# Kernel optimization log

Measured on AMD Instinct MI355X. Metric: run time of the kernel, lower is better.

Reference implementation:

```python
import jax, jax.numpy as jnp
import numpy as np

# NSA hyperparams (match init_kwargs)
D_BLK = 64    # d: block stride
L_CMP = 64    # compression block length (== d -> non-overlapping blocks)
L_SLC = 64    # selection block length (== l_cmp == d -> P_slc = P_cmp)
BQ = 64       # block_size_q
TOPK = 16     # slc_top_k
WL, WR = 512, 0  # sliding window (left, right)


def _nsa_forward(q, k, v, w_k, b_k, w_v, b_v, w_gate, b_gate, seqlen):
    S, qh, dim = q.shape
    kv = k.shape[1]
    H = qh // kv
    b = S // seqlen          # number of equal-length packed sequences
    s = seqlen
    scale = dim ** -0.5
    f32 = jnp.float32

    # [b, s, kv, H, e]: q head g*H+h belongs to kv head g (repeat_interleave layout)
    q5 = q.reshape(b, s, kv, H, dim)
    k3 = k.reshape(b, s, kv, dim)
    v3 = v.reshape(b, s, kv, dim)

    # ---- block compression (extract_blocks + cmp_linear over block length) ----
    n_blk = s // D_BLK
    kb = k.reshape(b, n_blk, D_BLK, kv, dim)
    vb = v.reshape(b, n_blk, D_BLK, kv, dim)
    K_cmp = jnp.einsum('bntke,t->bnke', kb, w_k) + b_k[0]
    V_cmp = jnp.einsum('bntke,t->bnke', vb, w_v) + b_v[0]

    # ---- compressed attention (per sequence, fp32 softmax) ----
    sc = jnp.einsum('bqkhe,bnke->bkhqn', q5, K_cmp).astype(f32) * scale
    P = jax.nn.softmax(sc, axis=-1)
    out_cmp = jnp.einsum('bkhqn,bnke->bqkhe', P.astype(q.dtype), V_cmp)

    # ---- selection scores: pool P over q-blocks and GQA groups, then top-k ----
    nqb = s // BQ
    pooled = P.reshape(b, kv, H, nqb, BQ, n_blk).sum(axis=(2, 4))  # [b,kv,nqb,n_blk]
    idx = jax.lax.top_k(pooled, TOPK)[1]                            # [b,kv,nqb,TOPK]

    # gather selected K/V blocks (shared by all queries in a q-block / GQA group)
    kb2 = jnp.transpose(kb, (0, 3, 1, 2, 4))  # [b,kv,n_blk,l,e]
    vb2 = jnp.transpose(vb, (0, 3, 1, 2, 4))
    gather = jax.vmap(jax.vmap(lambda blocks, i: blocks[i]))
    K_sel = gather(kb2, idx)  # [b,kv,nqb,TOPK,l,e]
    V_sel = gather(vb2, idx)

    # ---- selected-block attention ----
    qblk = q5.reshape(b, nqb, BQ, kv, H, dim)
    sc2 = jnp.einsum('bnckhe,bkntle->bkhnctl', qblk, K_sel).astype(f32) * scale
    sc2 = sc2.reshape(b, kv, H, nqb, BQ, TOPK * L_SLC)
    P2 = jax.nn.softmax(sc2, axis=-1).astype(q.dtype)
    out_slc = jnp.einsum('bkhncm,bknme->bnckhe', P2,
                         V_sel.reshape(b, kv, nqb, TOPK * L_SLC, dim))
    out_slc = out_slc.reshape(b, s, kv, H, dim)

    # ---- sliding-window attention (window_size=(WL, WR), non-causal flag) ----
    sw = jnp.einsum('bikhe,bjke->bkhij', q5, k3).astype(f32) * scale
    i = jnp.arange(s)[:, None]
    j = jnp.arange(s)[None, :]
    valid = (j >= i - WL) & (j <= i + WR)
    sw = jnp.where(valid, sw, -jnp.inf)
    Pw = jax.nn.softmax(sw, axis=-1).astype(q.dtype)
    out_win = jnp.einsum('bkhij,bjke->bikhe', Pw, v3)

    # ---- gated fusion of the three branches ----
    gate = jax.nn.sigmoid(jnp.einsum('bqkhe,ec->bqkhc', q5, w_gate) + b_gate)
    out = (gate[..., 0:1] * out_cmp
           + gate[..., 1:2] * out_slc
           + gate[..., 2:3] * out_win)
    return out.reshape(S, qh, dim)


def setup_inputs() -> dict:
    key = jax.random.key(0)
    ks = jax.random.split(key, 9)
    S, qh, kvh, dim = 4096, 8, 2, 128
    inp = {
        'q': jax.random.normal(ks[0], (S, qh, dim), jnp.float32),
        'k': jax.random.normal(ks[1], (S, kvh, dim), jnp.float32),
        'v': jax.random.normal(ks[2], (S, kvh, dim), jnp.float32),
        'w_k': jax.random.normal(ks[3], (L_CMP,), jnp.float32) * (L_CMP ** -0.5),
        'b_k': jax.random.normal(ks[4], (1,), jnp.float32) * 0.02,
        'w_v': jax.random.normal(ks[5], (L_CMP,), jnp.float32) * (L_CMP ** -0.5),
        'b_v': jax.random.normal(ks[6], (1,), jnp.float32) * 0.02,
        'w_gate': jax.random.normal(ks[7], (dim, 3), jnp.float32) * (dim ** -0.5),
        'b_gate': jax.random.normal(ks[8], (3,), jnp.float32) * 0.02,
        'seqlen': 2048,
    }
    return inp


def reference(q, k, v, w_k, b_k, w_v, b_v, w_gate, b_gate, seqlen):
    return _nsa_forward(q, k, v, w_k, b_k, w_v, b_v, w_gate, b_gate, seqlen)
```

## Files before the change

kernel.cpp:

```cpp
#include <hip/hip_runtime.h>
#include <hip/hip_bf16.h>


#define SEQ   2048
#define NB    2
#define KV    2
#define NH    4
#define QH    8
#define DIM   128
#define NBLK  32
#define NQB   32
#define NTOP  16
#define SCALE 0.08838834764831845f
#define QSC   0.12751831795244785f
#define VP    72
#define VSU   68

typedef unsigned short ushort_t;
using bf16x8 = __attribute__((ext_vector_type(8))) short;
using f32x4  = __attribute__((ext_vector_type(4))) float;

__device__ float g_slcB[4194304];
__device__ float g_winB[4194304];
__device__ float g_cp[1048576];
__device__ float g_mlg[4][65536];

__device__ __forceinline__ unsigned pkbf(float a, float b){
  union { __hip_bfloat162 h; unsigned u; } cv;
  cv.h = __float22bfloat162_rn(make_float2(a, b));
  return cv.u;
}
__device__ __forceinline__ ushort_t b16(float f){
  union { float f; unsigned i; } x; x.f = f;
  unsigned r = x.i + 0x7fffu + ((x.i >> 16) & 1u);
  return (ushort_t)(r >> 16);
}
__device__ __forceinline__ float fb(ushort_t h){
  union { unsigned i; float f; } x; x.i = ((unsigned)h) << 16;
  return x.f;
}

__global__ __launch_bounds__(256) void prep_k(
    const float* __restrict__ k, const float* __restrict__ v,
    const float* __restrict__ w_k, const float* __restrict__ b_k,
    const float* __restrict__ w_v, const float* __restrict__ b_v,
    ushort_t* __restrict__ Kb, ushort_t* __restrict__ VT,
    float* __restrict__ Kc, float* __restrict__ Vc)
{
  int blk = blockIdx.x;
  int db = blk & 1, rb = (blk >> 1) & 31, bbg = blk >> 6;
  int bb = bbg >> 1, g = bbg & 1;
  int tid = threadIdx.x;
  __shared__ ushort_t T[64*VP];
  __shared__ float wks[64], wvs[64];
  __shared__ float accK[16][64], accV[16][64];

  if (tid < 64){ wks[tid] = w_k[tid]; wvs[tid] = w_v[tid]; }
  __syncthreads();

  float4 sk = {0,0,0,0}, sv = {0,0,0,0};
  for (int jj = 0; jj < 4; ++jj){
    int i = tid + jj*256;
    int r = i >> 4, ds = i & 15;
    size_t src = ((size_t)(bb*SEQ + rb*64 + r)*KV + g)*DIM + db*64 + ds*4;
    float4 kx = *(const float4*)(k + src);
    float4 vx = *(const float4*)(v + src);
    uint2 kk; kk.x = pkbf(kx.x,kx.y); kk.y = pkbf(kx.z,kx.w);
    size_t rowb = ((size_t)bbg*SEQ + rb*64 + r)*DIM*2;
    int swz = (db*128 + ds*8) ^ ((r & 7) << 4);
    *(uint2*)((char*)Kb + rowb + swz) = kk;
    unsigned v01 = pkbf(vx.x,vx.y), v23 = pkbf(vx.z,vx.w);
    T[(ds*4+0)*VP + r] = (ushort_t)(v01 & 0xffffu);
    T[(ds*4+1)*VP + r] = (ushort_t)(v01 >> 16);
    T[(ds*4+2)*VP + r] = (ushort_t)(v23 & 0xffffu);
    T[(ds*4+3)*VP + r] = (ushort_t)(v23 >> 16);
    float a = wks[r], b = wvs[r];
    sk.x += a*kx.x; sk.y += a*kx.y; sk.z += a*kx.z; sk.w += a*kx.w;
    sv.x += b*vx.x; sv.y += b*vx.y; sv.z += b*vx.z; sv.w += b*vx.w;
  }
  *(float4*)&accK[tid>>4][(tid&15)*4] = sk;
  *(float4*)&accV[tid>>4][(tid&15)*4] = sv;
  __syncthreads();

  for (int jj = 0; jj < 4; ++jj){
    int i = tid + jj*256;
    int d = i >> 4, seg = i & 15;
    uint2 u = *(uint2*)&T[d*VP + seg*4];
    size_t rowb = ((size_t)bbg*DIM + db*64 + d)*SEQ*2;
    int swz = (seg*8) ^ ((d & 7) << 4);
    *(uint2*)((char*)VT + rowb + rb*128 + swz) = u;
  }

  size_t obase = ((size_t)(bbg*NBLK + rb))*DIM + db*64;
  if (tid < 64){
    float s = 0.f;
#pragma unroll
    for (int i = 0; i < 16; ++i) s += accK[i][tid];
    Kc[obase + tid] = s + b_k[0];
  } else if (tid < 128){
    int d = tid - 64;
    float s = 0.f;
#pragma unroll
    for (int i = 0; i < 16; ++i) s += accV[i][d];
    Vc[obase + d] = s + b_v[0];
  }
}

__global__ __launch_bounds__(512, 2) void attn_k(
    const float* __restrict__ q, const ushort_t* __restrict__ Kb,
    const ushort_t* __restrict__ VT, const float* __restrict__ Kc,
    const float* __restrict__ w_gate, const float* __restrict__ b_gate,
    float* __restrict__ slcbuf, float* __restrict__ out)
{
  int idx = blockIdx.x;
  int x = idx & 7, low = idx & 1, u = idx >> 3;
  int bbg = x >> 1;
  int j = u*2 + low;
  int role = j >> 6;
  int sub  = (j >> 5) & 1;
  int qb = j & 31;
  int bb = bbg >> 1, g = bbg & 1;

  int tid = threadIdx.x;
  int lane = tid & 63, w = tid >> 6;
  int quad = lane >> 4, l15 = lane & 15;
  int h = w & 3, qh2 = w >> 2;
  int xr = (l15 & 7) << 4;

  __shared__ ushort_t Ks[64*128];
  __shared__ ushort_t Vs[128*VSU];
  __shared__ ushort_t Ps[256*VP];
  __shared__ float pw[8][NBLK];
  __shared__ float gbuf[256];
  __shared__ int   idxs[NTOP];

  if (role == 0){
    int key = tid >> 4, dq = tid & 15;
    const float* kcs = Kc + ((size_t)bbg*NBLK + key)*DIM + dq*8;
    float4 f0 = *(const float4*)kcs, f1 = *(const float4*)(kcs + 4);
    float fe[8] = {f0.x,f0.y,f0.z,f0.w,f1.x,f1.y,f1.z,f1.w};
    union { ushort_t u[8]; uint4 v; } hi, lo;
#pragma unroll
    for (int e = 0; e < 8; ++e){
      ushort_t hh = b16(fe[e]);
      hi.u[e] = hh; lo.u[e] = b16(fe[e] - fb(hh));
    }
    int off = (dq*16) ^ ((key & 7) << 4);
    *(uint4*)((char*)&Ks[0] + key*256 + off) = hi.v;
    *(uint4*)((char*)&Ks[0] + (key+32)*256 + off) = lo.v;
  }

  const float* qrow0 = q + ((size_t)(bb*SEQ + qb*64 + qh2*32 + l15)*QH + g*NH + h)*DIM;
  const float* qrow1 = qrow0 + (size_t)16*QH*DIM;
  int gcol = 1 + role;
  bf16x8 qfrag0[4], qfrag1[4], qlo0[4], qlo1[4];
  float gp0 = 0.f, gp1 = 0.f, gc0 = 0.f, gc1 = 0.f;
#pragma unroll
  for (int kc = 0; kc < 4; ++kc){
    int d0 = kc*32 + quad*8;
    float4 a0 = *(const float4*)(qrow0 + d0);
    float4 a1 = *(const float4*)(qrow0 + d0 + 4);
    float4 b0 = *(const float4*)(qrow1 + d0);
    float4 b1 = *(const float4*)(qrow1 + d0 + 4);
    float qa[8] = {a0.x,a0.y,a0.z,a0.w,a1.x,a1.y,a1.z,a1.w};
    float qc[8] = {b0.x,b0.y,b0.z,b0.w,b1.x,b1.y,b1.z,b1.w};
#pragma unroll
    for (int jj = 0; jj < 8; ++jj){
      float wg = w_gate[(d0+jj)*3 + gcol];
      gp0 += qa[jj]*wg; gp1 += qc[jj]*wg;
    }
    if (role == 0){
#pragma unroll
      for (int jj = 0; jj < 8; ++jj){
        float w0 = w_gate[(d0+jj)*3];
        gc0 += qa[jj]*w0; gc1 += qc[jj]*w0;
      }
      union { ushort_t u[8]; bf16x8 v; } h0, l0, h1, l1;
#pragma unroll
      for (int e = 0; e < 8; ++e){
        float s0f = qa[e]*QSC; ushort_t hh0 = b16(s0f);
        h0.u[e] = hh0; l0.u[e] = b16(s0f - fb(hh0));
        float s1f = qc[e]*QSC; ushort_t hh1 = b16(s1f);
        h1.u[e] = hh1; l1.u[e] = b16(s1f - fb(hh1));
      }
      qfrag0[kc] = h0.v; qlo0[kc] = l0.v;
      qfrag1[kc] = h1.v; qlo1[kc] = l1.v;
    } else {
      union { unsigned uu[4]; bf16x8 v8; } t0, t1;
#pragma unroll
      for (int p2 = 0; p2 < 4; ++p2){
        t0.uu[p2] = pkbf(qa[2*p2]*QSC, qa[2*p2+1]*QSC);
        t1.uu[p2] = pkbf(qc[2*p2]*QSC, qc[2*p2+1]*QSC);
      }
      qfrag0[kc] = t0.v8; qfrag1[kc] = t1.v8;
    }
  }
  gp0 += __shfl_xor(gp0,16); gp0 += __shfl_xor(gp0,32);
  gp1 += __shfl_xor(gp1,16); gp1 += __shfl_xor(gp1,32);
  if (quad == 0){
    gbuf[w*32 + l15]      = 1.f/(1.f + __expf(-(gp0 + b_gate[gcol])));
    gbuf[w*32 + 16 + l15] = 1.f/(1.f + __expf(-(gp1 + b_gate[gcol])));
  }
  float g0c0 = 0.f, g0c1 = 0.f;
  if (role == 0){
    gc0 += __shfl_xor(gc0,16); gc0 += __shfl_xor(gc0,32);
    gc1 += __shfl_xor(gc1,16); gc1 += __shfl_xor(gc1,32);
    g0c0 = 1.f/(1.f + __expf(-(gc0 + b_gate[0])));
    g0c1 = 1.f/(1.f + __expf(-(gc1 + b_gate[0])));
  }
  __syncthreads();
  float gl0[4], gl1[4];
#pragma unroll
  for (int r = 0; r < 4; ++r){
    gl0[r] = gbuf[w*32 + quad*4 + r];
    gl1[r] = gbuf[w*32 + 16 + quad*4 + r];
  }

  const f32x4 zero4 = {0.f,0.f,0.f,0.f};

  if (role == 0){
    f32x4 c0[2], c1[2];
    c0[0]=zero4; c0[1]=zero4; c1[0]=zero4; c1[1]=zero4;
#pragma unroll
    for (int kc = 0; kc < 4; ++kc){
#pragma unroll
      for (int nt = 0; nt < 2; ++nt){
        bf16x8 ah = *(bf16x8*)((char*)&Ks[0] + (nt*16 + l15)*256
                               + ((kc*64 + quad*16) ^ xr));
        bf16x8 al = *(bf16x8*)((char*)&Ks[0] + (nt*16 + l15 + 32)*256
                               + ((kc*64 + quad*16) ^ xr));
        c0[nt] = __builtin_amdgcn_mfma_f32_16x16x32_bf16(ah, qfrag0[kc], c0[nt], 0, 0, 0);
        c0[nt] = __builtin_amdgcn_mfma_f32_16x16x32_bf16(ah, qlo0[kc],   c0[nt], 0, 0, 0);
        c0[nt] = __builtin_amdgcn_mfma_f32_16x16x32_bf16(al, qfrag0[kc], c0[nt], 0, 0, 0);
        c1[nt] = __builtin_amdgcn_mfma_f32_16x16x32_bf16(ah, qfrag1[kc], c1[nt], 0, 0, 0);
        c1[nt] = __builtin_amdgcn_mfma_f32_16x16x32_bf16(ah, qlo1[kc],   c1[nt], 0, 0, 0);
        c1[nt] = __builtin_amdgcn_mfma_f32_16x16x32_bf16(al, qfrag1[kc], c1[nt], 0, 0, 0);
      }
    }
    float mx0 = -INFINITY, mx1 = -INFINITY;
#pragma unroll
    for (int nt = 0; nt < 2; ++nt)
#pragma unroll
      for (int r = 0; r < 4; ++r){
        mx0 = fmaxf(mx0, c0[nt][r]); mx1 = fmaxf(mx1, c1[nt][r]);
      }
    mx0 = fmaxf(mx0, __shfl_xor(mx0,16)); mx0 = fmaxf(mx0, __shfl_xor(mx0,32));
    mx1 = fmaxf(mx1, __shfl_xor(mx1,16)); mx1 = fmaxf(mx1, __shfl_xor(mx1,32));
    float s0 = 0.f, s1 = 0.f;
#pragma unroll
    for (int nt = 0; nt < 2; ++nt)
#pragma unroll
      for (int r = 0; r < 4; ++r){
        float p0v = exp2f(c0[nt][r] - mx0); c0[nt][r] = p0v; s0 += p0v;
        float p1v = exp2f(c1[nt][r] - mx1); c1[nt][r] = p1v; s1 += p1v;
      }
    s0 += __shfl_xor(s0,16); s0 += __shfl_xor(s0,32);
    s1 += __shfl_xor(s1,16); s1 += __shfl_xor(s1,32);
    float ip0 = 1.f/s0, ip1 = 1.f/s1;
    if (sub == 0){
      float ig0 = g0c0*ip0, ig1 = g0c1*ip1;
      size_t rh0 = ((size_t)(bb*SEQ + qb*64 + qh2*32 + l15)*QH + g*NH + h);
      size_t rh1 = rh0 + (size_t)16*QH;
#pragma unroll
      for (int nt = 0; nt < 2; ++nt)
#pragma unroll
        for (int r = 0; r < 4; ++r){
          int key = nt*16 + quad*4 + r;
          g_cp[rh0*NBLK + key] = c0[nt][r]*ig0;
          g_cp[rh1*NBLK + key] = c1[nt][r]*ig1;
        }
    }
#pragma unroll
    for (int nt = 0; nt < 2; ++nt)
#pragma unroll
      for (int r = 0; r < 4; ++r){
        float t = c0[nt][r]*ip0 + c1[nt][r]*ip1;
        t += __shfl_xor(t,1); t += __shfl_xor(t,2);
        t += __shfl_xor(t,4); t += __shfl_xor(t,8);
        if (l15 == 0) pw[w][nt*16 + quad*4 + r] = t;
      }
    __syncthreads();
    if (tid < 64){
      int n = lane;
      float val = -INFINITY;
      if (n < NBLK){
        float sm = 0.f;
#pragma unroll
        for (int w2 = 0; w2 < 8; ++w2) sm += pw[w2][n];
        val = sm;
      }
      int idxv = n;
      for (int kk = 2; kk <= 32; kk <<= 1){
        for (int jj2 = kk >> 1; jj2 > 0; jj2 >>= 1){
          float pv = __shfl_xor(val, jj2);
          int   pi = __shfl_xor(idxv, jj2);
          bool lower = (lane & jj2) == 0;
          bool desc  = (lane & kk) == 0;
          bool iwin  = (val > pv) || (val == pv && idxv < pi);
          bool keep  = (lower == desc) ? iwin : !iwin;
          if (!keep){ val = pv; idxv = pi; }
        }
      }
      if (lane < NTOP) idxs[lane] = idxv;
    }
    __syncthreads();
  }

  const ushort_t* kbase  = Kb + (size_t)bbg*SEQ*DIM;
  const ushort_t* vtbase = VT + (size_t)bbg*DIM*SEQ;

  int kb0 = (qb >= 8) ? (qb - 8) : 0;
  int N   = qb - kb0 + 1;
  int nph0 = (N + 1) >> 1;
  int nph = (role == 0) ? 8 : (sub ? (N - nph0) : nph0);
  int tb  = kb0 + sub*nph0;
  int qi0 = qh2*32 + l15, qi1 = qi0 + 16;

  float m10 = -INFINITY, l10 = 0.f, m11 = -INFINITY, l11 = 0.f;
  f32x4 oacc0[8], oacc1[8];
#pragma unroll
  for (int dt = 0; dt < 8; ++dt){ oacc0[dt] = zero4; oacc1[dt] = zero4; }

  uint2 kr[4], vr[4];
  auto loadKV = [&](int rowbase){
#pragma unroll
    for (int jj = 0; jj < 4; ++jj){
      int unit = tid + jj*512;
      int krow = unit >> 5, kseg = unit & 31;
      kr[jj] = *(const uint2*)(kbase + (size_t)(rowbase + krow)*DIM + kseg*4);
      int vd = unit >> 4, vsg = unit & 15;
      vr[jj] = *(const uint2*)(vtbase + (size_t)vd*SEQ + rowbase + vsg*4);
    }
  };
  auto writeKV = [&](){
#pragma unroll
    for (int jj = 0; jj < 4; ++jj){
      int unit = tid + jj*512;
      int krow = unit >> 5, kseg = unit & 31;
      *(uint2*)&Ks[krow*128 + kseg*4] = kr[jj];
      int vd = unit >> 4, vsg = unit & 15;
      *(uint2*)&Vs[vd*VSU + vsg*4] = vr[jj];
    }
  };

  if (nph > 0){
    int r0 = (role == 0) ? idxs[sub*8]*64 : tb*64;
    loadKV(r0);
    writeKV();
    __syncthreads();

    for (int t = 0; t < nph; ++t){
      int kb = (role == 0) ? idxs[sub*8 + t] : (tb + t);
      if (t+1 < nph){
        int rn = (role == 0) ? idxs[sub*8 + t + 1]*64 : (tb + t + 1)*64;
        loadKV(rn);
      }
      __builtin_amdgcn_sched_barrier(0);

      f32x4 sacc0[4], sacc1[4];
#pragma unroll
      for (int nt = 0; nt < 4; ++nt){ sacc0[nt] = zero4; sacc1[nt] = zero4; }
      __builtin_amdgcn_s_setprio(1);
#pragma unroll
      for (int kc = 0; kc < 4; ++kc){
#pragma unroll
        for (int nt = 0; nt < 4; ++nt){
          bf16x8 a = *(bf16x8*)((char*)&Ks[0] + (nt*16 + l15)*256
                                + ((kc*64 + quad*16) ^ xr));
          sacc0[nt] = __builtin_amdgcn_mfma_f32_16x16x32_bf16(a, qfrag0[kc], sacc0[nt], 0, 0, 0);
          sacc1[nt] = __builtin_amdgcn_mfma_f32_16x16x32_bf16(a, qfrag1[kc], sacc1[nt], 0, 0, 0);
        }
      }
      __builtin_amdgcn_s_setprio(0);

      bool mlow  = (role == 1) && (qb >= 8) && (kb == qb - 8);
      bool mhigh = (role == 1) && (kb == qb);
      bool domask = mlow | mhigh;

      auto softmax_qt = [&](f32x4* sc2, float& m1r, float& l1r, int qi_l,
                            bool& skipped) -> float {
        if (domask){
#pragma unroll
          for (int nt = 0; nt < 4; ++nt)
#pragma unroll
            for (int r = 0; r < 4; ++r){
              int key = nt*16 + quad*4 + r;
              bool valid = (!mlow || key >= qi_l) && (!mhigh || key <= qi_l);
              sc2[nt][r] = valid ? sc2[nt][r] : -INFINITY;
            }
        }
        float mnt[4];
#pragma unroll
        for (int nt = 0; nt < 4; ++nt)
          mnt[nt] = fmaxf(fmaxf(sc2[nt][0], sc2[nt][1]),
                          fmaxf(sc2[nt][2], sc2[nt][3]));
        float mx = fmaxf(fmaxf(mnt[0], mnt[1]), fmaxf(mnt[2], mnt[3]));
        mx = fmaxf(mx, __shfl_xor(mx, 16));
        mx = fmaxf(mx, __shfl_xor(mx, 32));
        float al = 1.f;
        skipped = __all(mx <= m1r + 8.f);
        if (!skipped){
          float mn = fmaxf(m1r, mx);
          al = exp2f(m1r - mn);
          m1r = mn;
        }
        float snt[4];
#pragma unroll
        for (int nt = 0; nt < 4; ++nt){
          float p0 = exp2f(sc2[nt][0] - m1r);
          float p1 = exp2f(sc2[nt][1] - m1r);
          float p2 = exp2f(sc2[nt][2] - m1r);
          float p3 = exp2f(sc2[nt][3] - m1r);
          sc2[nt][0] = p0; sc2[nt][1] = p1; sc2[nt][2] = p2; sc2[nt][3] = p3;
          snt[nt] = (p0 + p1) + (p2 + p3);
        }
        float s0 = (snt[0] + snt[1]) + (snt[2] + snt[3]);
        s0 += __shfl_xor(s0, 16);
        s0 += __shfl_xor(s0, 32);
        l1r = l1r*al + s0;
        return al;
      };
      bool sk0, sk1;
      float al0 = softmax_qt(sacc0, m10, l10, qi0, sk0);
      float al1 = softmax_qt(sacc1, m11, l11, qi1, sk1);

#pragma unroll
      for (int nt = 0; nt < 4; ++nt){
        uint2 p0, p1;
        p0.x = pkbf(sacc0[nt][0], sacc0[nt][1]);
        p0.y = pkbf(sacc0[nt][2], sacc0[nt][3]);
        p1.x = pkbf(sacc1[nt][0], sacc1[nt][1]);
        p1.y = pkbf(sacc1[nt][2], sacc1[nt][3]);
        *(uint2*)&Ps[(w*32 + l15)*VP + nt*16 + quad*4] = p0;
        *(uint2*)&Ps[(w*32 + 16 + l15)*VP + nt*16 + quad*4] = p1;
      }

      if (!sk0){
        float ar[4];
#pragma unroll
        for (int r = 0; r < 4; ++r) ar[r] = __shfl(al0, quad*4 + r);
#pragma unroll
        for (int dt = 0; dt < 8; ++dt)
#pragma unroll
          for (int r = 0; r < 4; ++r) oacc0[dt][r] *= ar[r];
      }
      if (!sk1){
        float ar[4];
#pragma unroll
        for (int r = 0; r < 4; ++r) ar[r] = __shfl(al1, quad*4 + r);
#pragma unroll
        for (int dt = 0; dt < 8; ++dt)
#pragma unroll
          for (int r = 0; r < 4; ++r) oacc1[dt][r] *= ar[r];
      }

#pragma unroll
      for (int kc2 = 0; kc2 < 2; ++kc2){
        bf16x8 pa0 = *(bf16x8*)&Ps[(w*32 + l15)*VP + kc2*32 + quad*8];
        bf16x8 pa1 = *(bf16x8*)&Ps[(w*32 + 16 + l15)*VP + kc2*32 + quad*8];
        __builtin_amdgcn_s_setprio(1);
#pragma unroll
        for (int dt = 0; dt < 8; ++dt){
          bf16x8 vb8 = *(bf16x8*)((char*)&Vs[0] + (dt*16 + l15)*(VSU*2)
                                  + ((kc2*64 + quad*16) ^ xr));
          oacc0[dt] = __builtin_amdgcn_mfma_f32_16x16x32_bf16(pa0, vb8, oacc0[dt], 0, 0, 0);
          oacc1[dt] = __builtin_amdgcn_mfma_f32_16x16x32_bf16(pa1, vb8, oacc1[dt], 0, 0, 0);
        }
        __builtin_amdgcn_s_setprio(0);
      }

      if (t+1 < nph){
        __syncthreads();
        writeKV();
        __syncthreads();
      }
    }
  }

  int stream = role*2 + sub;
  float* obuf = (role == 0) ? (sub ? g_slcB : slcbuf)
                            : (sub ? g_winB : out);
#pragma unroll
  for (int r = 0; r < 4; ++r){
    float s20 = gl0[r];
    float s21 = gl1[r];
    size_t ob0 = ((size_t)(bb*SEQ + qb*64 + qh2*32 + quad*4 + r)*QH + g*NH + h)*DIM + l15;
    size_t ob1 = ob0 + (size_t)16*QH*DIM;
    float* op0 = obuf + ob0;
    float* op1 = obuf + ob1;
#pragma unroll
    for (int dt = 0; dt < 8; ++dt){
      op0[dt*16] = s20 * oacc0[dt][r];
      op1[dt*16] = s21 * oacc1[dt][r];
    }
  }
  if (quad == 0){
    size_t rh0 = ((size_t)(bb*SEQ + qb*64 + qh2*32 + l15)*QH + g*NH + h);
    size_t rh1 = rh0 + (size_t)16*QH;
    g_mlg[stream][rh0*2]     = m10;
    g_mlg[stream][rh0*2 + 1] = l10;
    g_mlg[stream][rh1*2]     = m11;
    g_mlg[stream][rh1*2 + 1] = l11;
  }
}

__global__ __launch_bounds__(256) void merge_k(
    const float* __restrict__ slcA, const float* __restrict__ Vc,
    float* __restrict__ out)
{
  int i = blockIdx.x * 256 + threadIdx.x;
  int rh = i >> 5;
  int d4 = (i & 31) * 4;

  float mA = g_mlg[0][rh*2], lA = g_mlg[0][rh*2+1];
  float mB = g_mlg[1][rh*2], lB = g_mlg[1][rh*2+1];
  float Ms = fmaxf(mA, mB);
  float wA = exp2f(mA - Ms), wB = exp2f(mB - Ms);
  float isl = 1.f/(lA*wA + lB*wB);
  float4 a4 = ((const float4*)slcA)[i];
  float4 b4 = ((const float4*)g_slcB)[i];
  float ox = (a4.x*wA + b4.x*wB)*isl;
  float oy = (a4.y*wA + b4.y*wB)*isl;
  float oz = (a4.z*wA + b4.z*wB)*isl;
  float ow = (a4.w*wA + b4.w*wB)*isl;

  float mC = g_mlg[2][rh*2], lC = g_mlg[2][rh*2+1];
  float mD = g_mlg[3][rh*2], lD = g_mlg[3][rh*2+1];
  float Mw = fmaxf(mC, mD);
  float wC = exp2f(mC - Mw), wD = exp2f(mD - Mw);
  float isw = 1.f/(lC*wC + lD*wD);
  float4 c4 = ((const float4*)out)[i];
  float4 e4 = ((const float4*)g_winB)[i];
  ox += (c4.x*wC + e4.x*wD)*isw;
  oy += (c4.y*wC + e4.y*wD)*isw;
  oz += (c4.z*wC + e4.z*wD)*isw;
  ow += (c4.w*wC + e4.w*wD)*isw;

  int row = rh >> 3, head = rh & 7;
  int bbg = (row >> 11)*2 + (head >> 2);
  const float* vc = Vc + ((size_t)bbg*NBLK)*DIM + d4;
  const float* cp = g_cp + (size_t)rh*NBLK;
  float cx = 0.f, cy = 0.f, cz = 0.f, cw = 0.f;
#pragma unroll 8
  for (int n = 0; n < NBLK; ++n){
    float p = cp[n];
    float4 v4 = *(const float4*)(vc + (size_t)n*DIM);
    cx += p*v4.x; cy += p*v4.y; cz += p*v4.z; cw += p*v4.w;
  }
  float4 o; o.x = ox + cx; o.y = oy + cy; o.z = oz + cz; o.w = ow + cw;
  ((float4*)out)[i] = o;
}

extern "C" void kernel_launch(void* const* d_in, const int* in_sizes, int n_in,
                              void* d_out, int out_size, void* d_ws, size_t ws_size,
                              hipStream_t stream) {
  const float* q      = (const float*)d_in[0];
  const float* k      = (const float*)d_in[1];
  const float* v      = (const float*)d_in[2];
  const float* w_k    = (const float*)d_in[3];
  const float* b_k    = (const float*)d_in[4];
  const float* w_v    = (const float*)d_in[5];
  const float* b_v    = (const float*)d_in[6];
  const float* w_gate = (const float*)d_in[7];
  const float* b_gate = (const float*)d_in[8];
  float* out = (float*)d_out;

  float* ws     = (float*)d_ws;
  float* Kc     = ws;
  float* Vc     = ws + 16384;
  float* slcbuf = ws + 49152;
  ushort_t* Kb  = (ushort_t*)(ws + 4243456);
  ushort_t* VT  = Kb + 1048576;

  prep_k <<<256, 256, 0, stream>>>(k, v, w_k, b_k, w_v, b_v, Kb, VT, Kc, Vc);
  attn_k <<<512, 512, 0, stream>>>(q, Kb, VT, Kc, w_gate, b_gate, slcbuf, out);
  merge_k<<<4096, 256, 0, stream>>>(slcbuf, Vc, out);
}
```

Measured before the change: 182.4 us.

## Stage K/V directly into LDS with async loads and double-buffer K tiles

```diff
diff --git a/kernel.cpp b/kernel.cpp
--- a/kernel.cpp
+++ b/kernel.cpp
@@ -14,7 +14,6 @@
 #define SCALE 0.08838834764831845f
 #define QSC   0.12751831795244785f
 #define VP    72
-#define VSU   68
 
 typedef unsigned short ushort_t;
 using bf16x8 = __attribute__((ext_vector_type(8))) short;
@@ -38,6 +37,13 @@
 __device__ __forceinline__ float fb(ushort_t h){
   union { unsigned i; float f; } x; x.i = ((unsigned)h) << 16;
   return x.f;
+}
+
+__device__ __forceinline__ void async16(ushort_t* l, const ushort_t* g){
+  __builtin_amdgcn_global_load_lds(
+      (const __attribute__((address_space(1))) unsigned int*)(size_t)g,
+      (__attribute__((address_space(3))) unsigned int*)(size_t)l,
+      16, 0, 0);
 }
 
 __global__ __launch_bounds__(256) void prep_k(
@@ -127,9 +133,9 @@
   int h = w & 3, qh2 = w >> 2;
   int xr = (l15 & 7) << 4;
 
-  __shared__ ushort_t Ks[64*128];
-  __shared__ ushort_t Vs[128*VSU];
-  __shared__ ushort_t Ps[256*VP];
+  __shared__ ushort_t Ks[2][64*128];
+  __shared__ ushort_t Vs[128*64];
+  __shared__ ushort_t Ps[128*VP];
   __shared__ float pw[8][NBLK];
   __shared__ float gbuf[256];
   __shared__ int   idxs[NTOP];
@@ -146,8 +152,8 @@
       hi.u[e] = hh; lo.u[e] = b16(fe[e] - fb(hh));
     }
     int off = (dq*16) ^ ((key & 7) << 4);
-    *(uint4*)((char*)&Ks[0] + key*256 + off) = hi.v;
-    *(uint4*)((char*)&Ks[0] + (key+32)*256 + off) = lo.v;
+    *(uint4*)((char*)&Ks[0][0] + key*256 + off) = hi.v;
+    *(uint4*)((char*)&Ks[0][0] + (key+32)*256 + off) = lo.v;
   }
 
   const float* qrow0 = q + ((size_t)(bb*SEQ + qb*64 + qh2*32 + l15)*QH + g*NH + h)*DIM;
@@ -225,9 +231,9 @@
     for (int kc = 0; kc < 4; ++kc){
 #pragma unroll
       for (int nt = 0; nt < 2; ++nt){
-        bf16x8 ah = *(bf16x8*)((char*)&Ks[0] + (nt*16 + l15)*256
+        bf16x8 ah = *(bf16x8*)((char*)&Ks[0][0] + (nt*16 + l15)*256
                                + ((kc*64 + quad*16) ^ xr));
-        bf16x8 al = *(bf16x8*)((char*)&Ks[0] + (nt*16 + l15 + 32)*256
+        bf16x8 al = *(bf16x8*)((char*)&Ks[0][0] + (nt*16 + l15 + 32)*256
                                + ((kc*64 + quad*16) ^ xr));
         c0[nt] = __builtin_amdgcn_mfma_f32_16x16x32_bf16(ah, qfrag0[kc], c0[nt], 0, 0, 0);
         c0[nt] = __builtin_amdgcn_mfma_f32_16x16x32_bf16(ah, qlo0[kc],   c0[nt], 0, 0, 0);
@@ -321,39 +327,33 @@
 #pragma unroll
   for (int dt = 0; dt < 8; ++dt){ oacc0[dt] = zero4; oacc1[dt] = zero4; }
 
-  uint2 kr[4], vr[4];
-  auto loadKV = [&](int rowbase){
-#pragma unroll
-    for (int jj = 0; jj < 4; ++jj){
-      int unit = tid + jj*512;
-      int krow = unit >> 5, kseg = unit & 31;
-      kr[jj] = *(const uint2*)(kbase + (size_t)(rowbase + krow)*DIM + kseg*4);
-      int vd = unit >> 4, vsg = unit & 15;
-      vr[jj] = *(const uint2*)(vtbase + (size_t)vd*SEQ + rowbase + vsg*4);
-    }
+  auto stageK = [&](int bufi, int rowbase){
+    const ushort_t* ksrc = kbase + (size_t)rowbase*DIM;
+#pragma unroll
+    for (int jj = 0; jj < 2; ++jj)
+      async16(&Ks[bufi][(jj*512 + w*64)*8], ksrc + (size_t)(tid + jj*512)*8);
   };
-  auto writeKV = [&](){
-#pragma unroll
-    for (int jj = 0; jj < 4; ++jj){
-      int unit = tid + jj*512;
-      int krow = unit >> 5, kseg = unit & 31;
-      *(uint2*)&Ks[krow*128 + kseg*4] = kr[jj];
-      int vd = unit >> 4, vsg = unit & 15;
-      *(uint2*)&Vs[vd*VSU + vsg*4] = vr[jj];
+  auto stageV = [&](int rowbase){
+    const ushort_t* vsrc = vtbase + rowbase;
+#pragma unroll
+    for (int jj = 0; jj < 2; ++jj){
+      int i = tid + jj*512;
+      int d = i >> 3, sg = i & 7;
+      async16(&Vs[(jj*512 + w*64)*8], vsrc + (size_t)d*SEQ + sg*8);
     }
   };
 
   if (nph > 0){
-    int r0 = (role == 0) ? idxs[sub*8]*64 : tb*64;
-    loadKV(r0);
-    writeKV();
-    __syncthreads();
+    stageK(0, (role == 0) ? idxs[sub*8]*64 : tb*64);
 
     for (int t = 0; t < nph; ++t){
+      int cur = t & 1;
       int kb = (role == 0) ? idxs[sub*8 + t] : (tb + t);
+      __syncthreads();
+      stageV(kb*64);
       if (t+1 < nph){
         int rn = (role == 0) ? idxs[sub*8 + t + 1]*64 : (tb + t + 1)*64;
-        loadKV(rn);
+        stageK(cur ^ 1, rn);
       }
       __builtin_amdgcn_sched_barrier(0);
 
@@ -365,7 +365,7 @@
       for (int kc = 0; kc < 4; ++kc){
 #pragma unroll
         for (int nt = 0; nt < 4; ++nt){
-          bf16x8 a = *(bf16x8*)((char*)&Ks[0] + (nt*16 + l15)*256
+          bf16x8 a = *(bf16x8*)((char*)&Ks[cur][0] + (nt*16 + l15)*256
                                 + ((kc*64 + quad*16) ^ xr));
           sacc0[nt] = __builtin_amdgcn_mfma_f32_16x16x32_bf16(a, qfrag0[kc], sacc0[nt], 0, 0, 0);
           sacc1[nt] = __builtin_amdgcn_mfma_f32_16x16x32_bf16(a, qfrag1[kc], sacc1[nt], 0, 0, 0);
@@ -424,25 +424,44 @@
       float al0 = softmax_qt(sacc0, m10, l10, qi0, sk0);
       float al1 = softmax_qt(sacc1, m11, l11, qi1, sk1);
 
+      asm volatile("s_waitcnt vmcnt(0)" ::: "memory");
+      __builtin_amdgcn_sched_barrier(0);
+
 #pragma unroll
       for (int nt = 0; nt < 4; ++nt){
-        uint2 p0, p1;
+        uint2 p0;
         p0.x = pkbf(sacc0[nt][0], sacc0[nt][1]);
         p0.y = pkbf(sacc0[nt][2], sacc0[nt][3]);
+        *(uint2*)&Ps[(w*16 + l15)*VP + nt*16 + quad*4] = p0;
+      }
+      if (!sk0){
+        float ar[4];
+#pragma unroll
+        for (int r = 0; r < 4; ++r) ar[r] = __shfl(al0, quad*4 + r);
+#pragma unroll
+        for (int dt = 0; dt < 8; ++dt)
+#pragma unroll
+          for (int r = 0; r < 4; ++r) oacc0[dt][r] *= ar[r];
+      }
+#pragma unroll
+      for (int kc2 = 0; kc2 < 2; ++kc2){
+        bf16x8 pa0 = *(bf16x8*)&Ps[(w*16 + l15)*VP + kc2*32 + quad*8];
+        __builtin_amdgcn_s_setprio(1);
+#pragma unroll
+        for (int dt = 0; dt < 8; ++dt){
+          bf16x8 vb8 = *(bf16x8*)((char*)&Vs[0] + (dt*16 + l15)*128
+                                  + ((kc2*64 + quad*16) ^ xr));
+          oacc0[dt] = __builtin_amdgcn_mfma_f32_16x16x32_bf16(pa0, vb8, oacc0[dt], 0, 0, 0);
+        }
+        __builtin_amdgcn_s_setprio(0);
+      }
+
+#pragma unroll
+      for (int nt = 0; nt < 4; ++nt){
+        uint2 p1;
         p1.x = pkbf(sacc1[nt][0], sacc1[nt][1]);
         p1.y = pkbf(sacc1[nt][2], sacc1[nt][3]);
-        *(uint2*)&Ps[(w*32 + l15)*VP + nt*16 + quad*4] = p0;
-        *(uint2*)&Ps[(w*32 + 16 + l15)*VP + nt*16 + quad*4] = p1;
-      }
-
-      if (!sk0){
-        float ar[4];
-#pragma unroll
-        for (int r = 0; r < 4; ++r) ar[r] = __shfl(al0, quad*4 + r);
-#pragma unroll
-        for (int dt = 0; dt < 8; ++dt)
-#pragma unroll
-          for (int r = 0; r < 4; ++r) oacc0[dt][r] *= ar[r];
+        *(uint2*)&Ps[(w*16 + l15)*VP + nt*16 + quad*4] = p1;
       }
       if (!sk1){
         float ar[4];
@@ -453,26 +472,17 @@
 #pragma unroll
           for (int r = 0; r < 4; ++r) oacc1[dt][r] *= ar[r];
       }
-
 #pragma unroll
       for (int kc2 = 0; kc2 < 2; ++kc2){
-        bf16x8 pa0 = *(bf16x8*)&Ps[(w*32 + l15)*VP + kc2*32 + quad*8];
-        bf16x8 pa1 = *(bf16x8*)&Ps[(w*32 + 16 + l15)*VP + kc2*32 + quad*8];
+        bf16x8 pa1 = *(bf16x8*)&Ps[(w*16 + l15)*VP + kc2*32 + quad*8];
         __builtin_amdgcn_s_setprio(1);
 #pragma unroll
         for (int dt = 0; dt < 8; ++dt){
-          bf16x8 vb8 = *(bf16x8*)((char*)&Vs[0] + (dt*16 + l15)*(VSU*2)
+          bf16x8 vb8 = *(bf16x8*)((char*)&Vs[0] + (dt*16 + l15)*128
                                   + ((kc2*64 + quad*16) ^ xr));
-          oacc0[dt] = __builtin_amdgcn_mfma_f32_16x16x32_bf16(pa0, vb8, oacc0[dt], 0, 0, 0);
           oacc1[dt] = __builtin_amdgcn_mfma_f32_16x16x32_bf16(pa1, vb8, oacc1[dt], 0, 0, 0);
         }
         __builtin_amdgcn_s_setprio(0);
-      }
-
-      if (t+1 < nph){
-        __syncthreads();
-        writeKV();
-        __syncthreads();
       }
     }
   }
```

Result: no change. 185.8 us (+1.9%).
